# Kernel tuning notes

Measured on AMD Instinct MI355X. Metric: run time of the kernel, lower is better.

The kernel has to match this reference:

```python
import jax, jax.numpy as jnp
import numpy as np

WEIGHT_GROUP = 128  # in-channel group size for scales (module default)


def setup_inputs() -> dict:
    key = jax.random.key(0)
    k1, k2, k3, k4, k5 = jax.random.split(key, 5)
    B, IN, OUT = 16, 8192, 8192
    nG = IN // WEIGHT_GROUP  # 64 scale groups along in_features
    x = jax.random.normal(k1, (B, IN), dtype=jnp.float32)
    # 'weight' stores the already-quantized low-bit float values (small magnitudes)
    weight = jax.random.normal(k2, (OUT, IN), dtype=jnp.float32)
    # per-(row, group) positive scales
    scale_buf = jax.random.uniform(k3, (OUT, nG), dtype=jnp.float32, minval=0.01, maxval=1.0)
    bias = jax.random.normal(k4, (1, OUT), dtype=jnp.float32)
    # per-[64, group]-block mantissa-format ids in {0,1,2}; selects the dequant
    # format on hardware but is a constant lookup (no float math) in the reference
    types = jax.random.randint(k5, (OUT // 64, nG), 0, 3, dtype=jnp.int32)
    return {"x": x, "weight": weight, "scale_buf": scale_buf, "bias": bias, "types": types}


def reference(x, weight, scale_buf, bias, types):
    O, I = weight.shape
    nG = scale_buf.shape[1]
    G = I // nG
    # group-wise dequant: w_deq[o, g*G + j] = weight[o, g*G + j] * scale_buf[o, g]
    w_deq = (weight.reshape(O, nG, G) * scale_buf[:, :, None]).reshape(O, I)
    # y = x @ W_deq^T + bias   [B, O]
    return jnp.einsum("bi,oi->bo", x, w_deq) + bias
```

## Files before the change

kernel.cpp:

```cpp
#include <hip/hip_runtime.h>
#include <hip/hip_bf16.h>

#define IN_F 8192
#define OUT_F 8192
#define NB 16
#define NG 64
#define KSPLIT 16
#define KRANGE (IN_F / KSPLIT)
#define BK 256
#define NCHUNK (KRANGE / BK)
#define NSTEP (KRANGE / 32)
#define WSTRIDE 264

typedef __attribute__((ext_vector_type(8))) short bf16x8;
typedef __attribute__((ext_vector_type(4))) float f32x4;

static __device__ __forceinline__ unsigned bfpack2(float a, float b) {
    unsigned ua = __float_as_uint(a) + 0x8000u;
    unsigned ub = __float_as_uint(b) + 0x8000u;
    return __builtin_amdgcn_perm(ub, ua, 0x07060302u);
}

__global__ __launch_bounds__(256)
void init_out_kernel(const float* __restrict__ bias, float* __restrict__ out) {
    const int i = blockIdx.x * 256 + threadIdx.x;
    out[i] = bias[i & (OUT_F - 1)];
}

__global__ __launch_bounds__(256, 3)
void axcore_mfma_kernel(const float* __restrict__ x,
                        const float* __restrict__ w,
                        const float* __restrict__ scale,
                        float* __restrict__ out) {
    __shared__ __align__(16) unsigned short xswz[NSTEP * 64 * 8];
    __shared__ __align__(16) unsigned short wlds[64 * WSTRIDE];

    const int t    = threadIdx.x;
    const int wv   = t >> 6;
    const int lane = t & 63;
    const int k0   = blockIdx.y * KRANGE;
    const int ob   = blockIdx.x * 64;
    const int o0   = ob + wv * 16;

#pragma unroll
    for (int p = 0; p < 8; ++p) {
        const int idx = p * 256 + t;
        const int m   = idx >> 7;
        const int k4  = (idx & 127) * 4;
        const float4 v = *(const float4*)&x[m * IN_F + k0 + k4];
        const int tt = k4 >> 5;
        const int ln = m + 16 * ((k4 & 31) >> 3);
        const int jj = k4 & 7;
        uint2 sv;
        sv.x = bfpack2(v.x, v.y);
        sv.y = bfpack2(v.z, v.w);
        *(uint2*)&xswz[(tt * 64 + ln) * 8 + jj] = sv;
    }

    f32x4 acc = {0.f, 0.f, 0.f, 0.f};
    const int nrow = o0 + (lane & 15);

#pragma unroll
    for (int c = 0; c < NCHUNK; ++c) {
        if (c > 0) __syncthreads();

        const int kcg = k0 + c * BK;
        const int gb  = kcg >> 7;
#pragma unroll
        for (int i = 0; i < 16; ++i) {
            const int rl  = wv * 16 + i;
            const int row = ob + rl;
            const float4 v = *(const float4*)&w[(size_t)row * IN_F + kcg + 4 * lane];
            const float s = scale[row * NG + gb + (lane >> 5)];
            uint2 pk;
            pk.x = bfpack2(v.x * s, v.y * s);
            pk.y = bfpack2(v.z * s, v.w * s);
            *(uint2*)&wlds[rl * WSTRIDE + lane * 4] = pk;
        }
        __syncthreads();

#pragma unroll
        for (int tl = 0; tl < BK / 32; ++tl) {
            const int ts = c * (BK / 32) + tl;
            const bf16x8 afrag = *(const bf16x8*)&xswz[(ts * 64 + lane) * 8];
            const bf16x8 bfrag = *(const bf16x8*)
                &wlds[(wv * 16 + (lane & 15)) * WSTRIDE + tl * 32 + (lane >> 4) * 8];
            acc = __builtin_amdgcn_mfma_f32_16x16x32_bf16(afrag, bfrag, acc, 0, 0, 0);
        }
    }

#pragma unroll
    for (int r = 0; r < 4; ++r) {
        const int b = (lane >> 4) * 4 + r;
        atomicAdd(&out[b * OUT_F + nrow], acc[r]);
    }
}

extern "C" void kernel_launch(void* const* d_in, const int* in_sizes, int n_in,
                              void* d_out, int out_size, void* d_ws, size_t ws_size,
                              hipStream_t stream) {
    const float* x    = (const float*)d_in[0];
    const float* w    = (const float*)d_in[1];
    const float* sc   = (const float*)d_in[2];
    const float* bias = (const float*)d_in[3];
    float* out = (float*)d_out;

    hipLaunchKernelGGL(init_out_kernel, dim3(NB * OUT_F / 256), dim3(256),
                       0, stream, bias, out);
    hipLaunchKernelGGL(axcore_mfma_kernel, dim3(OUT_F / 64, KSPLIT), dim3(256),
                       0, stream, x, w, sc, out);
}
```

Measured before the change: 373.8 us.

## Stream weights directly into MFMA B-fragments, dropping LDS staging of W

Each lane now loads its weight fragment (two float4 per 32-wide k-step) straight from global memory, scales and packs it to bf16 in registers, and feeds it to the MFMA. This removes the LDS round trip and the per-chunk barriers for W. KSPLIT is halved, which doubles the x slice staged in LDS and halves the atomic adds, and the occupancy hint rises to 4. The trade-off is less coalesced weight loads: each lane reads 32 contiguous bytes per row, spread across 16 rows. Fewer k-split blocks also means less parallelism.

```diff
diff --git a/kernel.cpp b/kernel.cpp
--- a/kernel.cpp
+++ b/kernel.cpp
@@ -1,16 +1,13 @@
 #include <hip/hip_runtime.h>
-#include <hip/hip_bf16.h>
 
 #define IN_F 8192
 #define OUT_F 8192
 #define NB 16
 #define NG 64
-#define KSPLIT 16
+#define KSPLIT 8
 #define KRANGE (IN_F / KSPLIT)
-#define BK 256
-#define NCHUNK (KRANGE / BK)
 #define NSTEP (KRANGE / 32)
-#define WSTRIDE 264
+#define GPB (KRANGE / 128)
 
 typedef __attribute__((ext_vector_type(8))) short bf16x8;
 typedef __attribute__((ext_vector_type(4))) float f32x4;
@@ -27,13 +24,12 @@
     out[i] = bias[i & (OUT_F - 1)];
 }
 
-__global__ __launch_bounds__(256, 3)
-void axcore_mfma_kernel(const float* __restrict__ x,
-                        const float* __restrict__ w,
-                        const float* __restrict__ scale,
-                        float* __restrict__ out) {
+__global__ __launch_bounds__(256, 4)
+void axcore_stream_kernel(const float* __restrict__ x,
+                          const float* __restrict__ w,
+                          const float* __restrict__ scale,
+                          float* __restrict__ out) {
     __shared__ __align__(16) unsigned short xswz[NSTEP * 64 * 8];
-    __shared__ __align__(16) unsigned short wlds[64 * WSTRIDE];
 
     const int t    = threadIdx.x;
     const int wv   = t >> 6;
@@ -43,10 +39,10 @@
     const int o0   = ob + wv * 16;
 
 #pragma unroll
-    for (int p = 0; p < 8; ++p) {
+    for (int p = 0; p < 16; ++p) {
         const int idx = p * 256 + t;
-        const int m   = idx >> 7;
-        const int k4  = (idx & 127) * 4;
+        const int m   = idx >> 8;
+        const int k4  = (idx & 255) * 4;
         const float4 v = *(const float4*)&x[m * IN_F + k0 + k4];
         const int tt = k4 >> 5;
         const int ln = m + 16 * ((k4 & 31) >> 3);
@@ -56,36 +52,32 @@
         sv.y = bfpack2(v.z, v.w);
         *(uint2*)&xswz[(tt * 64 + ln) * 8 + jj] = sv;
     }
+    __syncthreads();
+
+    const int nrow = o0 + (lane & 15);
+    const int koff = (lane >> 4) * 8;
+    const float* wp = w + (size_t)nrow * IN_F + k0 + koff;
+    const float* sp = scale + nrow * NG + blockIdx.y * GPB;
 
     f32x4 acc = {0.f, 0.f, 0.f, 0.f};
-    const int nrow = o0 + (lane & 15);
 
+#pragma unroll 2
+    for (int g = 0; g < GPB; ++g) {
+        const float s = sp[g];
 #pragma unroll
-    for (int c = 0; c < NCHUNK; ++c) {
-        if (c > 0) __syncthreads();
-
-        const int kcg = k0 + c * BK;
-        const int gb  = kcg >> 7;
-#pragma unroll
-        for (int i = 0; i < 16; ++i) {
-            const int rl  = wv * 16 + i;
-            const int row = ob + rl;
-            const float4 v = *(const float4*)&w[(size_t)row * IN_F + kcg + 4 * lane];
-            const float s = scale[row * NG + gb + (lane >> 5)];
-            uint2 pk;
-            pk.x = bfpack2(v.x * s, v.y * s);
-            pk.y = bfpack2(v.z * s, v.w * s);
-            *(uint2*)&wlds[rl * WSTRIDE + lane * 4] = pk;
-        }
-        __syncthreads();
-
-#pragma unroll
-        for (int tl = 0; tl < BK / 32; ++tl) {
-            const int ts = c * (BK / 32) + tl;
+        for (int u = 0; u < 4; ++u) {
+            const int ts = g * 4 + u;
+            const float4 f0 = *(const float4*)(wp + ts * 32);
+            const float4 f1 = *(const float4*)(wp + ts * 32 + 4);
+            uint4 pk;
+            pk.x = bfpack2(f0.x * s, f0.y * s);
+            pk.y = bfpack2(f0.z * s, f0.w * s);
+            pk.z = bfpack2(f1.x * s, f1.y * s);
+            pk.w = bfpack2(f1.z * s, f1.w * s);
+            union { uint4 u4; bf16x8 h; } cv;
+            cv.u4 = pk;
             const bf16x8 afrag = *(const bf16x8*)&xswz[(ts * 64 + lane) * 8];
-            const bf16x8 bfrag = *(const bf16x8*)
-                &wlds[(wv * 16 + (lane & 15)) * WSTRIDE + tl * 32 + (lane >> 4) * 8];
-            acc = __builtin_amdgcn_mfma_f32_16x16x32_bf16(afrag, bfrag, acc, 0, 0, 0);
+            acc = __builtin_amdgcn_mfma_f32_16x16x32_bf16(afrag, cv.h, acc, 0, 0, 0);
         }
     }
 
@@ -107,6 +99,6 @@
 
     hipLaunchKernelGGL(init_out_kernel, dim3(NB * OUT_F / 256), dim3(256),
                        0, stream, bias, out);
-    hipLaunchKernelGGL(axcore_mfma_kernel, dim3(OUT_F / 64, KSPLIT), dim3(256),
+    hipLaunchKernelGGL(axcore_stream_kernel, dim3(OUT_F / 64, KSPLIT), dim3(256),
                        0, stream, x, w, sc, out);
 }
```

After: 379.3 us. No clear change (+1.5%).
